# Performance work log

Measured on AMD Instinct MI355X. Metric: run time of the kernel, lower is better.

The kernel has to match this reference:

```python
import jax, jax.numpy as jnp
import numpy as np

N = 131072          # batch rows
D = 3               # number of feature dims (one small MLP per dim)
H = 128             # hidden width == inter_dim (hidden_sizes[0])


def setup_inputs() -> dict:
    key = jax.random.key(0)
    ks = jax.random.split(key, 12)
    x = jax.random.normal(ks[0], (N, D), dtype=jnp.float32)
    mask = jax.random.bernoulli(ks[1], 0.5, (N, D))
    s = 1.0 / np.sqrt(H)
    # Per-dim MLP: 1 -> 128 -> 128 -> 128 -> 128 (ReLU between layers).
    # Stack the 3 per-dim networks along a leading D axis.
    W0 = jax.random.normal(ks[2], (D, H), dtype=jnp.float32)            # in_dim = 1
    b0 = jax.random.normal(ks[3], (D, H), dtype=jnp.float32) * s
    W1 = jax.random.normal(ks[4], (D, H, H), dtype=jnp.float32) * s
    b1 = jax.random.normal(ks[5], (D, H), dtype=jnp.float32) * s
    W2 = jax.random.normal(ks[6], (D, H, H), dtype=jnp.float32) * s
    b2 = jax.random.normal(ks[7], (D, H), dtype=jnp.float32) * s
    W3 = jax.random.normal(ks[8], (D, H, H), dtype=jnp.float32) * s
    b3 = jax.random.normal(ks[9], (D, H), dtype=jnp.float32) * s
    return {"x": x, "mask": mask, "W0": W0, "b0": b0, "W1": W1, "b1": b1,
            "W2": W2, "b2": b2, "W3": W3, "b3": b3}


def reference(x, mask, W0, b0, W1, b1, W2, b2, W3, b3):
    # Vectorized equivalent of the per-dim gather -> MLP -> scatter loop:
    # unmasked rows contribute zeros (out is initialized to zeros and only
    # idx = where(mask[:, dim]) rows are written), so masked-multiply is exact.
    h = jax.nn.relu(x[:, :, None] * W0[None] + b0[None])          # [N, D, H]
    h = jax.nn.relu(jnp.einsum('ndh,dhk->ndk', h, W1) + b1[None])
    h = jax.nn.relu(jnp.einsum('ndh,dhk->ndk', h, W2) + b2[None])
    o = jnp.einsum('ndh,dhk->ndk', h, W3) + b3[None]              # [N, D, H]
    o = o * mask[:, :, None].astype(o.dtype)
    return jnp.sum(o, axis=1)                                     # [N, H]
```

## Files before the change

### kernel.cpp

```cpp
#include <hip/hip_runtime.h>
#include <hip/hip_bf16.h>
#include <cstdint>

#define HD 128

typedef __attribute__((ext_vector_type(8))) short short8;
typedef __attribute__((ext_vector_type(4))) float f32x4;
typedef __attribute__((ext_vector_type(4))) unsigned int u32x4;

static __device__ __forceinline__ short bf16_bits(float v) {
    __hip_bfloat16 h = __float2bfloat16(v);
    return __builtin_bit_cast(short, h);
}

__global__ void detect_mask_kernel(const unsigned char* __restrict__ mask,
                                   int n_elems, int* __restrict__ flag)
{
    __shared__ int any;
    if (threadIdx.x == 0) any = 0;
    __syncthreads();
    int limit = n_elems / 4;
    if (limit > 4096) limit = 4096;
    int local = 0;
    for (int k = threadIdx.x; k < limit; k += blockDim.x)
        local |= mask[4 * k + 1];
    if (local) atomicOr(&any, 1);
    __syncthreads();
    if (threadIdx.x == 0) *flag = any;
}

__global__ __launch_bounds__(256) void precast_kernel(
    const float* __restrict__ W1, const float* __restrict__ W2,
    const float* __restrict__ W3, char* __restrict__ ws)
{
    const int s = blockIdx.x;
    const int d = s / 3, li = s % 3;
    const float* W = (li == 0 ? W1 : li == 1 ? W2 : W3) + d * HD * HD;
    const int t = threadIdx.x;
    const int p = blockIdx.y * 4 + (t >> 6);
    const int l = t & 63;
    const int kb = p >> 3, tm = p & 7;
    const int g = l >> 4;
    const int m = tm * 16 + (l & 15);
    const int jbase = 32 * kb + 4 * g;
    unsigned int pk[4];
    #pragma unroll
    for (int w = 0; w < 4; ++w) {
        const int j0 = jbase + (w >> 1) * 16 + (w & 1) * 2;
        const float a = W[j0 * HD + m];
        const float b = W[(j0 + 1) * HD + m];
        pk[w] = (unsigned short)bf16_bits(a) |
                ((unsigned)(unsigned short)bf16_bits(b) << 16);
    }
    *reinterpret_cast<u32x4*>(ws + s * 32768 + p * 1024 + l * 16) =
        u32x4{pk[0], pk[1], pk[2], pk[3]};
}

static __device__ __forceinline__ void stage_weights(const char* __restrict__ src,
                                                     char* ldsdst, int wid, int lane)
{
    #pragma unroll
    for (int it = 0; it < 8; ++it) {
        const int c = wid * 8 + it;
        __builtin_amdgcn_global_load_lds(
            (const __attribute__((address_space(1))) void*)(src + c * 1024 + lane * 16),
            (__attribute__((address_space(3))) void*)(ldsdst + c * 1024),
            16, 0, 0);
    }
}

__global__ __launch_bounds__(256, 2) void mlp_kernel(
    const float* __restrict__ x, const void* __restrict__ maskraw,
    const int* __restrict__ mflag,
    const float* __restrict__ W0, const float* __restrict__ b0,
    const float* __restrict__ b1, const float* __restrict__ b2,
    const float* __restrict__ b3, const char* __restrict__ wsWT,
    float* __restrict__ out)
{
    __shared__ char wlds[2 * 32768];
    const int tid  = threadIdx.x;
    const int wid  = tid >> 6;
    const int lane = tid & 63;
    const int r    = lane & 15;
    const int g    = lane >> 4;
    const int row0 = blockIdx.x * 128 + wid * 32;
    const bool bytewise = (*mflag != 0);
    const unsigned char* mask_b = (const unsigned char*)maskraw;
    const int*           mask_w = (const int*)maskraw;

    f32x4 acc3[8][2];
    #pragma unroll
    for (int tm = 0; tm < 8; ++tm)
        #pragma unroll
        for (int tc = 0; tc < 2; ++tc)
            acc3[tm][tc] = f32x4{0.f, 0.f, 0.f, 0.f};

    stage_weights(wsWT, wlds, wid, lane);

    short8 bfrag[4][2];
    f32x4  acct[8][2];
    int cur = 0;

    for (int d = 0; d < 3; ++d) {
        float xv[2], mkf[2];
        #pragma unroll
        for (int tc = 0; tc < 2; ++tc) {
            const int mi = (row0 + tc * 16 + r) * 3 + d;
            xv[tc]  = x[mi];
            mkf[tc] = (bytewise ? (mask_b[mi] != 0) : (mask_w[mi] != 0)) ? 1.0f : 0.0f;
        }

        const float* W0d = W0 + d * HD;
        const float* b0d = b0 + d * HD;
        #pragma unroll
        for (int kb = 0; kb < 4; ++kb) {
            const f32x4 w0a = *(const f32x4*)(W0d + kb * 32 + g * 4);
            const f32x4 w0b = *(const f32x4*)(W0d + kb * 32 + 16 + g * 4);
            const f32x4 bba = *(const f32x4*)(b0d + kb * 32 + g * 4);
            const f32x4 bbb = *(const f32x4*)(b0d + kb * 32 + 16 + g * 4);
            #pragma unroll
            for (int tc = 0; tc < 2; ++tc) {
                short8 f;
                #pragma unroll
                for (int q = 0; q < 4; ++q) {
                    const float va = fmaxf(xv[tc] * w0a[q] + bba[q], 0.f);
                    const float vb = fmaxf(xv[tc] * w0b[q] + bbb[q], 0.f);
                    f[q]     = bf16_bits(va);
                    f[4 + q] = bf16_bits(vb);
                }
                bfrag[kb][tc] = f;
            }
        }

        #pragma unroll
        for (int li = 0; li < 3; ++li) {
            const int s = d * 3 + li;
            __syncthreads();
            if (s < 8) stage_weights(wsWT + (s + 1) * 32768, wlds + (cur ^ 1) * 32768, wid, lane);
            const char* wbase = wlds + cur * 32768;

            if (li < 2) {
                const float* bb = (li == 0 ? b1 : b2) + d * HD;
                #pragma unroll
                for (int tm = 0; tm < 8; ++tm) {
                    const f32x4 bv = *(const f32x4*)(bb + tm * 16 + g * 4);
                    #pragma unroll
                    for (int tc = 0; tc < 2; ++tc) acct[tm][tc] = bv;
                }
            }

            #pragma unroll
            for (int kb = 0; kb < 4; ++kb) {
                short8 afr[8];
                #pragma unroll
                for (int tm = 0; tm < 8; ++tm)
                    afr[tm] = *reinterpret_cast<const short8*>(
                        wbase + (kb * 8 + tm) * 1024 + lane * 16);
                #pragma unroll
                for (int tm = 0; tm < 8; ++tm)
                    #pragma unroll
                    for (int tc = 0; tc < 2; ++tc) {
                        if (li < 2)
                            acct[tm][tc] = __builtin_amdgcn_mfma_f32_16x16x32_bf16(
                                afr[tm], bfrag[kb][tc], acct[tm][tc], 0, 0, 0);
                        else
                            acc3[tm][tc] = __builtin_amdgcn_mfma_f32_16x16x32_bf16(
                                afr[tm], bfrag[kb][tc], acc3[tm][tc], 0, 0, 0);
                    }
            }

            if (li < 2) {
                #pragma unroll
                for (int kb = 0; kb < 4; ++kb)
                    #pragma unroll
                    for (int tc = 0; tc < 2; ++tc) {
                        short8 f;
                        #pragma unroll
                        for (int q = 0; q < 4; ++q) {
                            float va = fmaxf(acct[2 * kb][tc][q], 0.f);
                            float vb = fmaxf(acct[2 * kb + 1][tc][q], 0.f);
                            if (li == 1) { va *= mkf[tc]; vb *= mkf[tc]; }
                            f[q]     = bf16_bits(va);
                            f[4 + q] = bf16_bits(vb);
                        }
                        bfrag[kb][tc] = f;
                    }
            }
            cur ^= 1;
        }
    }

    #pragma unroll
    for (int tc = 0; tc < 2; ++tc) {
        const int row = row0 + tc * 16 + r;
        float mk[3];
        #pragma unroll
        for (int dd = 0; dd < 3; ++dd) {
            const int mi = row * 3 + dd;
            mk[dd] = (bytewise ? (mask_b[mi] != 0) : (mask_w[mi] != 0)) ? 1.f : 0.f;
        }
        float* orow = out + (long)row * HD;
        #pragma unroll
        for (int tm = 0; tm < 8; ++tm) {
            const f32x4 ba  = *(const f32x4*)(b3 + 0 * HD + tm * 16 + g * 4);
            const f32x4 bbv = *(const f32x4*)(b3 + 1 * HD + tm * 16 + g * 4);
            const f32x4 bc  = *(const f32x4*)(b3 + 2 * HD + tm * 16 + g * 4);
            f32x4 o = acc3[tm][tc];
            #pragma unroll
            for (int q = 0; q < 4; ++q)
                o[q] += mk[0] * ba[q] + mk[1] * bbv[q] + mk[2] * bc[q];
            *reinterpret_cast<f32x4*>(orow + tm * 16 + g * 4) = o;
        }
    }
}

extern "C" void kernel_launch(void* const* d_in, const int* in_sizes, int n_in,
                              void* d_out, int out_size, void* d_ws, size_t ws_size,
                              hipStream_t stream) {
    const float* x  = (const float*)d_in[0];
    const unsigned char* mask = (const unsigned char*)d_in[1];
    const float* W0 = (const float*)d_in[2];
    const float* b0 = (const float*)d_in[3];
    const float* W1 = (const float*)d_in[4];
    const float* b1 = (const float*)d_in[5];
    const float* W2 = (const float*)d_in[6];
    const float* b2 = (const float*)d_in[7];
    const float* W3 = (const float*)d_in[8];
    const float* b3 = (const float*)d_in[9];
    float* out = (float*)d_out;
    char* ws = (char*)d_ws;
    int* mflag = (int*)(ws + 9 * 32768);
    const int n_mask = in_sizes[1];

    hipLaunchKernelGGL(detect_mask_kernel, dim3(1), dim3(256), 0, stream,
                       mask, n_mask, mflag);
    hipLaunchKernelGGL(precast_kernel, dim3(9, 8), dim3(256), 0, stream, W1, W2, W3, ws);
    hipLaunchKernelGGL(mlp_kernel, dim3(1024), dim3(256), 0, stream,
                       x, (const void*)mask, mflag, W0, b0, b1, b2, b3, ws, out);
}
```

Baseline: 143.5 us.

## Single-buffer weight LDS, restructure MFMA loops for occupancy, fuse mask detect

The mask-format detection kernel is folded into the first block of the weight precast kernel, which removes one launch. The MLP kernel drops from a double-buffered 64KB LDS weight buffer to a single 32KB buffer and raises launch bounds to 3 blocks per CU. The layer loops are restructured so each pair of output tiles is finished and converted before moving on, which shrinks live accumulator registers. The cost is that weight staging is no longer overlapped with compute inside a block: each layer now waits on a full sync-load-sync sequence and relies on other resident blocks to hide that latency.

```diff
diff --git a/kernel.cpp b/kernel.cpp
--- a/kernel.cpp
+++ b/kernel.cpp
@@ -13,26 +13,24 @@
     return __builtin_bit_cast(short, h);
 }
 
-__global__ void detect_mask_kernel(const unsigned char* __restrict__ mask,
-                                   int n_elems, int* __restrict__ flag)
-{
-    __shared__ int any;
-    if (threadIdx.x == 0) any = 0;
-    __syncthreads();
-    int limit = n_elems / 4;
-    if (limit > 4096) limit = 4096;
-    int local = 0;
-    for (int k = threadIdx.x; k < limit; k += blockDim.x)
-        local |= mask[4 * k + 1];
-    if (local) atomicOr(&any, 1);
-    __syncthreads();
-    if (threadIdx.x == 0) *flag = any;
-}
-
 __global__ __launch_bounds__(256) void precast_kernel(
     const float* __restrict__ W1, const float* __restrict__ W2,
-    const float* __restrict__ W3, char* __restrict__ ws)
+    const float* __restrict__ W3, const unsigned char* __restrict__ mask,
+    int n_mask, char* __restrict__ ws, int* __restrict__ mflag)
 {
+    if (blockIdx.x == 0 && blockIdx.y == 0) {
+        __shared__ int any;
+        if (threadIdx.x == 0) any = 0;
+        __syncthreads();
+        int limit = n_mask / 4;
+        if (limit > 4096) limit = 4096;
+        int local = 0;
+        for (int k = threadIdx.x; k < limit; k += 256)
+            local |= mask[4 * k + 1];
+        if (local) atomicOr(&any, 1);
+        __syncthreads();
+        if (threadIdx.x == 0) *mflag = any;
+    }
     const int s = blockIdx.x;
     const int d = s / 3, li = s % 3;
     const float* W = (li == 0 ? W1 : li == 1 ? W2 : W3) + d * HD * HD;
@@ -56,20 +54,68 @@
         u32x4{pk[0], pk[1], pk[2], pk[3]};
 }
 
-static __device__ __forceinline__ void stage_weights(const char* __restrict__ src,
-                                                     char* ldsdst, int wid, int lane)
+static __device__ __forceinline__ void stage_img(const char* __restrict__ src,
+                                                 char* dst, int tid)
 {
     #pragma unroll
-    for (int it = 0; it < 8; ++it) {
-        const int c = wid * 8 + it;
+    for (int it = 0; it < 8; ++it)
         __builtin_amdgcn_global_load_lds(
-            (const __attribute__((address_space(1))) void*)(src + c * 1024 + lane * 16),
-            (__attribute__((address_space(3))) void*)(ldsdst + c * 1024),
+            (const __attribute__((address_space(1))) void*)(src + it * 4096 + tid * 16),
+            (__attribute__((address_space(3))) void*)(dst + it * 4096 + tid * 16),
             16, 0, 0);
-    }
-}
-
-__global__ __launch_bounds__(256, 2) void mlp_kernel(
+}
+
+#define MFMA16(A, B, C) __builtin_amdgcn_mfma_f32_16x16x32_bf16(A, B, C, 0, 0, 0)
+
+#define LAYER_MID(BSRC, BDST, BIAS, FOLDM)                                    \
+  {                                                                           \
+    _Pragma("unroll")                                                         \
+    for (int pm = 0; pm < 4; ++pm) {                                          \
+      f32x4 aA0, aA1, aB0, aB1;                                               \
+      {                                                                       \
+        const f32x4 bvA = *(const f32x4*)((BIAS) + (2 * pm) * 16 + g * 4);    \
+        const f32x4 bvB = *(const f32x4*)((BIAS) + (2 * pm + 1) * 16 + g * 4);\
+        aA0 = bvA; aA1 = bvA; aB0 = bvB; aB1 = bvB;                           \
+      }                                                                       \
+      _Pragma("unroll")                                                       \
+      for (int kb = 0; kb < 4; ++kb) {                                        \
+        const short8 a0 = *(const short8*)(wlds + (kb * 8 + 2 * pm) * 1024 + lofs);     \
+        const short8 a1 = *(const short8*)(wlds + (kb * 8 + 2 * pm + 1) * 1024 + lofs); \
+        aA0 = MFMA16(a0, BSRC[kb][0], aA0);                                   \
+        aA1 = MFMA16(a0, BSRC[kb][1], aA1);                                   \
+        aB0 = MFMA16(a1, BSRC[kb][0], aB0);                                   \
+        aB1 = MFMA16(a1, BSRC[kb][1], aB1);                                   \
+      }                                                                       \
+      _Pragma("unroll")                                                       \
+      for (int q = 0; q < 4; ++q) {                                           \
+        float vA0 = fmaxf(aA0[q], 0.f), vA1 = fmaxf(aA1[q], 0.f);             \
+        float vB0 = fmaxf(aB0[q], 0.f), vB1 = fmaxf(aB1[q], 0.f);             \
+        if (FOLDM) { vA0 *= mkf0; vA1 *= mkf1; vB0 *= mkf0; vB1 *= mkf1; }    \
+        BDST[pm][0][q]     = bf16_bits(vA0);                                  \
+        BDST[pm][0][4 + q] = bf16_bits(vB0);                                  \
+        BDST[pm][1][q]     = bf16_bits(vA1);                                  \
+        BDST[pm][1][4 + q] = bf16_bits(vB1);                                  \
+      }                                                                       \
+    }                                                                         \
+  }
+
+#define LAYER_FIN(BSRC)                                                       \
+  {                                                                           \
+    _Pragma("unroll")                                                         \
+    for (int pm = 0; pm < 4; ++pm) {                                          \
+      _Pragma("unroll")                                                       \
+      for (int kb = 0; kb < 4; ++kb) {                                        \
+        const short8 a0 = *(const short8*)(wlds + (kb * 8 + 2 * pm) * 1024 + lofs);     \
+        const short8 a1 = *(const short8*)(wlds + (kb * 8 + 2 * pm + 1) * 1024 + lofs); \
+        acc3[2 * pm][0]     = MFMA16(a0, BSRC[kb][0], acc3[2 * pm][0]);       \
+        acc3[2 * pm][1]     = MFMA16(a0, BSRC[kb][1], acc3[2 * pm][1]);       \
+        acc3[2 * pm + 1][0] = MFMA16(a1, BSRC[kb][0], acc3[2 * pm + 1][0]);   \
+        acc3[2 * pm + 1][1] = MFMA16(a1, BSRC[kb][1], acc3[2 * pm + 1][1]);   \
+      }                                                                       \
+    }                                                                         \
+  }
+
+__global__ __launch_bounds__(256, 3) void mlp_kernel(
     const float* __restrict__ x, const void* __restrict__ maskraw,
     const int* __restrict__ mflag,
     const float* __restrict__ W0, const float* __restrict__ b0,
@@ -77,12 +123,13 @@
     const float* __restrict__ b3, const char* __restrict__ wsWT,
     float* __restrict__ out)
 {
-    __shared__ char wlds[2 * 32768];
+    __shared__ char wlds[32768];
     const int tid  = threadIdx.x;
     const int wid  = tid >> 6;
     const int lane = tid & 63;
     const int r    = lane & 15;
     const int g    = lane >> 4;
+    const int lofs = lane * 16;
     const int row0 = blockIdx.x * 128 + wid * 32;
     const bool bytewise = (*mflag != 0);
     const unsigned char* mask_b = (const unsigned char*)maskraw;
@@ -95,99 +142,54 @@
         for (int tc = 0; tc < 2; ++tc)
             acc3[tm][tc] = f32x4{0.f, 0.f, 0.f, 0.f};
 
-    stage_weights(wsWT, wlds, wid, lane);
-
-    short8 bfrag[4][2];
-    f32x4  acct[8][2];
-    int cur = 0;
+    short8 bfA[4][2], bfB[4][2];
+
+    stage_img(wsWT, wlds, tid);
 
     for (int d = 0; d < 3; ++d) {
-        float xv[2], mkf[2];
-        #pragma unroll
-        for (int tc = 0; tc < 2; ++tc) {
-            const int mi = (row0 + tc * 16 + r) * 3 + d;
-            xv[tc]  = x[mi];
-            mkf[tc] = (bytewise ? (mask_b[mi] != 0) : (mask_w[mi] != 0)) ? 1.0f : 0.0f;
-        }
-
-        const float* W0d = W0 + d * HD;
-        const float* b0d = b0 + d * HD;
-        #pragma unroll
-        for (int kb = 0; kb < 4; ++kb) {
-            const f32x4 w0a = *(const f32x4*)(W0d + kb * 32 + g * 4);
-            const f32x4 w0b = *(const f32x4*)(W0d + kb * 32 + 16 + g * 4);
-            const f32x4 bba = *(const f32x4*)(b0d + kb * 32 + g * 4);
-            const f32x4 bbb = *(const f32x4*)(b0d + kb * 32 + 16 + g * 4);
+        const int mi0 = (row0 + r) * 3 + d;
+        const int mi1 = (row0 + 16 + r) * 3 + d;
+        const float xv0 = x[mi0], xv1 = x[mi1];
+        const float mkf0 = (bytewise ? (mask_b[mi0] != 0) : (mask_w[mi0] != 0)) ? 1.f : 0.f;
+        const float mkf1 = (bytewise ? (mask_b[mi1] != 0) : (mask_w[mi1] != 0)) ? 1.f : 0.f;
+
+        {
+            const float* W0d = W0 + d * HD;
+            const float* b0d = b0 + d * HD;
             #pragma unroll
-            for (int tc = 0; tc < 2; ++tc) {
-                short8 f;
+            for (int kb = 0; kb < 4; ++kb) {
+                const f32x4 w0a = *(const f32x4*)(W0d + kb * 32 + g * 4);
+                const f32x4 w0b = *(const f32x4*)(W0d + kb * 32 + 16 + g * 4);
+                const f32x4 bba = *(const f32x4*)(b0d + kb * 32 + g * 4);
+                const f32x4 bbb = *(const f32x4*)(b0d + kb * 32 + 16 + g * 4);
                 #pragma unroll
-                for (int q = 0; q < 4; ++q) {
-                    const float va = fmaxf(xv[tc] * w0a[q] + bba[q], 0.f);
-                    const float vb = fmaxf(xv[tc] * w0b[q] + bbb[q], 0.f);
-                    f[q]     = bf16_bits(va);
-                    f[4 + q] = bf16_bits(vb);
+                for (int tc = 0; tc < 2; ++tc) {
+                    const float xx = tc ? xv1 : xv0;
+                    short8 f;
+                    #pragma unroll
+                    for (int q = 0; q < 4; ++q) {
+                        f[q]     = bf16_bits(fmaxf(xx * w0a[q] + bba[q], 0.f));
+                        f[4 + q] = bf16_bits(fmaxf(xx * w0b[q] + bbb[q], 0.f));
+                    }
+                    bfA[kb][tc] = f;
                 }
-                bfrag[kb][tc] = f;
             }
         }
 
-        #pragma unroll
-        for (int li = 0; li < 3; ++li) {
-            const int s = d * 3 + li;
-            __syncthreads();
-            if (s < 8) stage_weights(wsWT + (s + 1) * 32768, wlds + (cur ^ 1) * 32768, wid, lane);
-            const char* wbase = wlds + cur * 32768;
-
-            if (li < 2) {
-                const float* bb = (li == 0 ? b1 : b2) + d * HD;
-                #pragma unroll
-                for (int tm = 0; tm < 8; ++tm) {
-                    const f32x4 bv = *(const f32x4*)(bb + tm * 16 + g * 4);
-                    #pragma unroll
-                    for (int tc = 0; tc < 2; ++tc) acct[tm][tc] = bv;
-                }
-            }
-
-            #pragma unroll
-            for (int kb = 0; kb < 4; ++kb) {
-                short8 afr[8];
-                #pragma unroll
-                for (int tm = 0; tm < 8; ++tm)
-                    afr[tm] = *reinterpret_cast<const short8*>(
-                        wbase + (kb * 8 + tm) * 1024 + lane * 16);
-                #pragma unroll
-                for (int tm = 0; tm < 8; ++tm)
-                    #pragma unroll
-                    for (int tc = 0; tc < 2; ++tc) {
-                        if (li < 2)
-                            acct[tm][tc] = __builtin_amdgcn_mfma_f32_16x16x32_bf16(
-                                afr[tm], bfrag[kb][tc], acct[tm][tc], 0, 0, 0);
-                        else
-                            acc3[tm][tc] = __builtin_amdgcn_mfma_f32_16x16x32_bf16(
-                                afr[tm], bfrag[kb][tc], acc3[tm][tc], 0, 0, 0);
-                    }
-            }
-
-            if (li < 2) {
-                #pragma unroll
-                for (int kb = 0; kb < 4; ++kb)
-                    #pragma unroll
-                    for (int tc = 0; tc < 2; ++tc) {
-                        short8 f;
-                        #pragma unroll
-                        for (int q = 0; q < 4; ++q) {
-                            float va = fmaxf(acct[2 * kb][tc][q], 0.f);
-                            float vb = fmaxf(acct[2 * kb + 1][tc][q], 0.f);
-                            if (li == 1) { va *= mkf[tc]; vb *= mkf[tc]; }
-                            f[q]     = bf16_bits(va);
-                            f[4 + q] = bf16_bits(vb);
-                        }
-                        bfrag[kb][tc] = f;
-                    }
-            }
-            cur ^= 1;
-        }
+        __syncthreads();
+        LAYER_MID(bfA, bfB, b1 + d * HD, false);
+        __syncthreads();
+        stage_img(wsWT + (d * 3 + 1) * 32768, wlds, tid);
+
+        __syncthreads();
+        LAYER_MID(bfB, bfA, b2 + d * HD, true);
+        __syncthreads();
+        stage_img(wsWT + (d * 3 + 2) * 32768, wlds, tid);
+
+        __syncthreads();
+        LAYER_FIN(bfA);
+        __syncthreads();
+        if (d < 2) stage_img(wsWT + (d * 3 + 3) * 32768, wlds, tid);
     }
 
     #pragma unroll
@@ -232,9 +234,8 @@
     int* mflag = (int*)(ws + 9 * 32768);
     const int n_mask = in_sizes[1];
 
-    hipLaunchKernelGGL(detect_mask_kernel, dim3(1), dim3(256), 0, stream,
-                       mask, n_mask, mflag);
-    hipLaunchKernelGGL(precast_kernel, dim3(9, 8), dim3(256), 0, stream, W1, W2, W3, ws);
+    hipLaunchKernelGGL(precast_kernel, dim3(9, 8), dim3(256), 0, stream,
+                       W1, W2, W3, mask, n_mask, ws, mflag);
     hipLaunchKernelGGL(mlp_kernel, dim3(1024), dim3(256), 0, stream,
                        x, (const void*)mask, mflag, W0, b0, b1, b2, b3, ws, out);
 }
```

New measurement: 148.4 us. +3.4%, slower.
